# Optimization experiments

Hardware: AMD Instinct MI355X
Metric: run time of the kernel (lower is better)

## Reference

```python
import jax, jax.numpy as jnp
import numpy as np

TEMPERATURE = 0.6


def setup_inputs() -> dict:
    key = jax.random.key(0)
    k1, k2, k3 = jax.random.split(key, 3)
    B, IN, OUT, C = 8192, 256, 32, 50
    x = jax.random.uniform(k1, (B, IN), dtype=jnp.float32)
    weight = jax.random.normal(k2, (C, OUT, IN), dtype=jnp.float32) * 0.05
    bias = jax.random.normal(k3, (C, 1, OUT), dtype=jnp.float32) * 0.05
    return {"x": x, "weight": weight, "bias": bias}


def reference(x, weight, bias):
    # gamma[c,i] = L1 norm of weight over out dim: sum_o |W[c,o,i]|
    gamma = jnp.sum(jnp.abs(weight), axis=1)            # [C, IN]
    alpha = jax.nn.softmax(gamma / TEMPERATURE, axis=1)  # [C, IN]
    alpha_norm = alpha / jnp.max(alpha, axis=1, keepdims=True)  # [C, IN]
    # gated input per class: [C, B, IN]
    xg = x[None, :, :] * alpha_norm[:, None, :]
    # per-class GEMM: y[c,b,o] = sum_i xg[c,b,i] * W[c,o,i]
    y = jnp.einsum('cbi,coi->cbo', xg, weight) + bias    # [C, B, OUT]
    return jnp.transpose(y, (1, 0, 2))                   # [B, C, OUT]
```

## Files before the change

### kernel.cpp

```cpp
#include <hip/hip_runtime.h>
#include <hip/hip_bf16.h>

typedef __bf16 bf16x8 __attribute__((ext_vector_type(8)));
typedef float  f32x4  __attribute__((ext_vector_type(4)));

#define B_ROWS 8192
#define IN_DIM 256
#define OUT_DIM 32
#define NCLS 50
#define INV_T (1.0f / 0.6f)

#define CVT_BLOCKS 1024
#define GBLOCKS 512

__device__ __forceinline__ void gload_lds16(const void* g, void* l) {
    __builtin_amdgcn_global_load_lds(
        (const __attribute__((address_space(1))) void*)g,
        (__attribute__((address_space(3))) void*)l, 16, 0, 0);
}

__global__ __launch_bounds__(256) void prep(const float* __restrict__ x,
                                            const float* __restrict__ w,
                                            __bf16* __restrict__ xb,
                                            __bf16* __restrict__ wb) {
    __shared__ float wm[4];
    int bid = blockIdx.x;
    if (bid < CVT_BLOCKS) {
        int i = (bid * 256 + threadIdx.x) * 8;
        float4 v0 = *reinterpret_cast<const float4*>(x + i);
        float4 v1 = *reinterpret_cast<const float4*>(x + i + 4);
        bf16x8 r;
        r[0] = (__bf16)v0.x; r[1] = (__bf16)v0.y; r[2] = (__bf16)v0.z; r[3] = (__bf16)v0.w;
        r[4] = (__bf16)v1.x; r[5] = (__bf16)v1.y; r[6] = (__bf16)v1.z; r[7] = (__bf16)v1.w;
        *reinterpret_cast<bf16x8*>(xb + i) = r;
    } else {
        int c = bid - CVT_BLOCKS;
        int i = threadIdx.x;
        const float* wc = w + (size_t)c * OUT_DIM * IN_DIM;
        float g = 0.f;
#pragma unroll
        for (int o = 0; o < OUT_DIM; ++o) g += fabsf(wc[o * IN_DIM + i]);
        float m = g;
#pragma unroll
        for (int s = 1; s < 64; s <<= 1) m = fmaxf(m, __shfl_xor(m, s));
        if ((threadIdx.x & 63) == 0) wm[threadIdx.x >> 6] = m;
        __syncthreads();
        m = fmaxf(fmaxf(wm[0], wm[1]), fmaxf(wm[2], wm[3]));
        float an = __expf((g - m) * INV_T);
        __bf16* wbc = wb + (size_t)c * OUT_DIM * IN_DIM;
#pragma unroll
        for (int o = 0; o < OUT_DIM; ++o)
            wbc[o * IN_DIM + i] = (__bf16)(wc[o * IN_DIM + i] * an);
    }
}

__global__ __launch_bounds__(256, 2) void gemm(const __bf16* __restrict__ xb,
                                               const __bf16* __restrict__ wb,
                                               const float* __restrict__ bias,
                                               float* __restrict__ out) {
    __shared__ __align__(16) char lds[4 * 2 * 8192];

    int bid = blockIdx.x;
    int p = (bid * 25) >> 9;
    int first = (p * GBLOCKS + 24) / 25;
    int next  = ((p + 1) * GBLOCKS + 24) / 25;
    int j = bid - first;
    int np = next - first;
    int u0 = (j * 128) / np;
    int u1 = ((j + 1) * 128) / np;
    int nch = u1 - u0;

    int c0 = p * 2;
    int lane = threadIdx.x & 63;
    int w4 = threadIdx.x >> 6;
    int l15 = lane & 15;
    int g = lane >> 4;
    int s31 = lane & 31;
    int lr = lane >> 5;

    char* Abuf0 = lds + w4 * 16384;
    char* Abuf1 = Abuf0 + 8192;

    const char* arows = (const char*)(xb + (size_t)(u0 * 64 + w4 * 16) * IN_DIM);
#define STAGE_A(BUF, AP)                                                          \
    _Pragma("unroll") for (int il = 0; il < 8; ++il) {                            \
        int r = 2 * il + lr;                                                      \
        gload_lds16((AP) + (size_t)r * 512 + ((s31 ^ r) * 16),                    \
                    (BUF) + il * 1024);                                           \
    }
    STAGE_A(Abuf0, arows)

    const char* wsrc = (const char*)(wb + (size_t)c0 * OUT_DIM * IN_DIM);
#pragma unroll
    for (int jw = 0; jw < 8; ++jw) {
        int re = jw * 8 + w4 * 2;
        int r = re + lr;
        gload_lds16(wsrc + (size_t)r * 512 + ((s31 ^ (r & 15)) * 16),
                    lds + (re >> 4) * 16384 + 8192 + (re & 15) * 512);
    }

    asm volatile("s_waitcnt vmcnt(0)" ::: "memory");
    __syncthreads();
    __builtin_amdgcn_sched_barrier(0);

    bf16x8 W[2][16];
#pragma unroll
    for (int ci = 0; ci < 2; ++ci)
#pragma unroll
        for (int kk = 0; kk < 8; ++kk) {
            int slot = (4 * kk + g) ^ l15;
            W[ci][kk]     = *reinterpret_cast<const bf16x8*>(
                lds + (2 * ci) * 16384 + 8192 + l15 * 512 + slot * 16);
            W[ci][8 + kk] = *reinterpret_cast<const bf16x8*>(
                lds + (2 * ci + 1) * 16384 + 8192 + l15 * 512 + slot * 16);
        }
#pragma unroll
    for (int ci = 0; ci < 2; ++ci)
#pragma unroll
        for (int kk = 0; kk < 16; ++kk)
            asm volatile("" : "+v"(W[ci][kk]));
    __builtin_amdgcn_sched_barrier(0);
    __syncthreads();

    float4 bv00 = *reinterpret_cast<const float4*>(bias + c0 * OUT_DIM + g * 4);
    float4 bv01 = *reinterpret_cast<const float4*>(bias + c0 * OUT_DIM + 16 + g * 4);
    float4 bv10 = *reinterpret_cast<const float4*>(bias + (c0 + 1) * OUT_DIM + g * 4);
    float4 bv11 = *reinterpret_cast<const float4*>(bias + (c0 + 1) * OUT_DIM + 16 + g * 4);

    float* orow = out + (size_t)(u0 * 64 + w4 * 16 + l15) * (NCLS * OUT_DIM) + c0 * OUT_DIM + g * 4;

    char* cur = Abuf0;
    char* nxt = Abuf1;
    const char* anext = arows + 64 * 512;

    for (int k = 0; k < nch; ++k) {
        if (k + 1 < nch) {
            STAGE_A(nxt, anext)
            asm volatile("s_waitcnt vmcnt(12)" ::: "memory");
        } else {
            asm volatile("s_waitcnt vmcnt(4)" ::: "memory");
        }
        __builtin_amdgcn_sched_barrier(0);

        f32x4 acc00 = {bv00.x, bv00.y, bv00.z, bv00.w};
        f32x4 acc01 = {bv01.x, bv01.y, bv01.z, bv01.w};
        f32x4 acc10 = {bv10.x, bv10.y, bv10.z, bv10.w};
        f32x4 acc11 = {bv11.x, bv11.y, bv11.z, bv11.w};
#pragma unroll
        for (int kk = 0; kk < 8; ++kk) {
            int slot = (4 * kk + g) ^ l15;
            bf16x8 a = *reinterpret_cast<const bf16x8*>(cur + (size_t)l15 * 512 + slot * 16);
            acc00 = __builtin_amdgcn_mfma_f32_16x16x32_bf16(W[0][kk],     a, acc00, 0, 0, 0);
            acc01 = __builtin_amdgcn_mfma_f32_16x16x32_bf16(W[0][8 + kk], a, acc01, 0, 0, 0);
            acc10 = __builtin_amdgcn_mfma_f32_16x16x32_bf16(W[1][kk],     a, acc10, 0, 0, 0);
            acc11 = __builtin_amdgcn_mfma_f32_16x16x32_bf16(W[1][8 + kk], a, acc11, 0, 0, 0);
        }
        *reinterpret_cast<f32x4*>(orow) = acc00;
        *reinterpret_cast<f32x4*>(orow + 16) = acc01;
        *reinterpret_cast<f32x4*>(orow + OUT_DIM) = acc10;
        *reinterpret_cast<f32x4*>(orow + OUT_DIM + 16) = acc11;

        char* t = cur; cur = nxt; nxt = t;
        anext += 64 * 512;
        orow += (size_t)64 * (NCLS * OUT_DIM);
    }
#undef STAGE_A
}

extern "C" void kernel_launch(void* const* d_in, const int* in_sizes, int n_in,
                              void* d_out, int out_size, void* d_ws, size_t ws_size,
                              hipStream_t stream) {
    const float* x    = (const float*)d_in[0];
    const float* w    = (const float*)d_in[1];
    const float* bias = (const float*)d_in[2];
    float* out = (float*)d_out;

    __bf16* xb = (__bf16*)d_ws;
    __bf16* wb = xb + (size_t)B_ROWS * IN_DIM;

    prep<<<CVT_BLOCKS + NCLS, 256, 0, stream>>>(x, w, xb, wb);
    gemm<<<GBLOCKS, 256, 0, stream>>>(xb, wb, bias, out);
}
```

Measured before the change: 32.83 us.

## Load weights directly to registers and prefetch two A tiles up front

The prep kernel now schedules the weight-gating blocks first so they start early, and it loads each weight column into registers once instead of reading it twice. The GEMM kernel loads its weight fragments straight from global memory into registers, which removes the LDS staging round trip and two block barriers. It also issues the first two A-tile prefetches before the first compute, so more loads overlap with the MFMA work. The risk is that uncoalesced per-lane weight loads and higher register pressure could offset these savings.

```diff
diff --git a/kernel.cpp b/kernel.cpp
--- a/kernel.cpp
+++ b/kernel.cpp
@@ -25,32 +25,35 @@
                                             __bf16* __restrict__ wb) {
     __shared__ float wm[4];
     int bid = blockIdx.x;
-    if (bid < CVT_BLOCKS) {
-        int i = (bid * 256 + threadIdx.x) * 8;
+    if (bid < NCLS) {
+        int c = bid;
+        int i = threadIdx.x;
+        const float* wc = w + (size_t)c * OUT_DIM * IN_DIM + i;
+        float wv[OUT_DIM];
+#pragma unroll
+        for (int o = 0; o < OUT_DIM; ++o) wv[o] = wc[o * IN_DIM];
+        float gsum = 0.f;
+#pragma unroll
+        for (int o = 0; o < OUT_DIM; ++o) gsum += fabsf(wv[o]);
+        float m = gsum;
+#pragma unroll
+        for (int s = 1; s < 64; s <<= 1) m = fmaxf(m, __shfl_xor(m, s));
+        if ((threadIdx.x & 63) == 0) wm[threadIdx.x >> 6] = m;
+        __syncthreads();
+        m = fmaxf(fmaxf(wm[0], wm[1]), fmaxf(wm[2], wm[3]));
+        float an = __expf((gsum - m) * INV_T);
+        __bf16* wo = wb + (size_t)c * OUT_DIM * IN_DIM + i;
+#pragma unroll
+        for (int o = 0; o < OUT_DIM; ++o)
+            wo[o * IN_DIM] = (__bf16)(wv[o] * an);
+    } else {
+        int i = ((bid - NCLS) * 256 + threadIdx.x) * 8;
         float4 v0 = *reinterpret_cast<const float4*>(x + i);
         float4 v1 = *reinterpret_cast<const float4*>(x + i + 4);
         bf16x8 r;
         r[0] = (__bf16)v0.x; r[1] = (__bf16)v0.y; r[2] = (__bf16)v0.z; r[3] = (__bf16)v0.w;
         r[4] = (__bf16)v1.x; r[5] = (__bf16)v1.y; r[6] = (__bf16)v1.z; r[7] = (__bf16)v1.w;
         *reinterpret_cast<bf16x8*>(xb + i) = r;
-    } else {
-        int c = bid - CVT_BLOCKS;
-        int i = threadIdx.x;
-        const float* wc = w + (size_t)c * OUT_DIM * IN_DIM;
-        float g = 0.f;
-#pragma unroll
-        for (int o = 0; o < OUT_DIM; ++o) g += fabsf(wc[o * IN_DIM + i]);
-        float m = g;
-#pragma unroll
-        for (int s = 1; s < 64; s <<= 1) m = fmaxf(m, __shfl_xor(m, s));
-        if ((threadIdx.x & 63) == 0) wm[threadIdx.x >> 6] = m;
-        __syncthreads();
-        m = fmaxf(fmaxf(wm[0], wm[1]), fmaxf(wm[2], wm[3]));
-        float an = __expf((g - m) * INV_T);
-        __bf16* wbc = wb + (size_t)c * OUT_DIM * IN_DIM;
-#pragma unroll
-        for (int o = 0; o < OUT_DIM; ++o)
-            wbc[o * IN_DIM + i] = (__bf16)(wc[o * IN_DIM + i] * an);
     }
 }
 
@@ -81,6 +84,29 @@
     char* Abuf0 = lds + w4 * 16384;
     char* Abuf1 = Abuf0 + 8192;
 
+    const __bf16* wp = wb + ((size_t)c0 * OUT_DIM + l15) * IN_DIM + g * 8;
+    bf16x8 W[2][16];
+#pragma unroll
+    for (int ci = 0; ci < 2; ++ci)
+#pragma unroll
+        for (int kk = 0; kk < 8; ++kk) {
+            W[ci][kk]     = *reinterpret_cast<const bf16x8*>(wp + ci * 32 * IN_DIM + kk * 32);
+            W[ci][8 + kk] = *reinterpret_cast<const bf16x8*>(wp + (ci * 32 + 16) * IN_DIM + kk * 32);
+        }
+    f32x4 bv00 = *reinterpret_cast<const f32x4*>(bias + c0 * OUT_DIM + g * 4);
+    f32x4 bv01 = *reinterpret_cast<const f32x4*>(bias + c0 * OUT_DIM + 16 + g * 4);
+    f32x4 bv10 = *reinterpret_cast<const f32x4*>(bias + (c0 + 1) * OUT_DIM + g * 4);
+    f32x4 bv11 = *reinterpret_cast<const f32x4*>(bias + (c0 + 1) * OUT_DIM + 16 + g * 4);
+
+#pragma unroll
+    for (int ci = 0; ci < 2; ++ci)
+#pragma unroll
+        for (int kk = 0; kk < 16; ++kk)
+            asm volatile("" : "+v"(W[ci][kk]));
+    asm volatile("" : "+v"(bv00), "+v"(bv01), "+v"(bv10), "+v"(bv11));
+    asm volatile("s_waitcnt vmcnt(0)" ::: "memory");
+    __builtin_amdgcn_sched_barrier(0);
+
     const char* arows = (const char*)(xb + (size_t)(u0 * 64 + w4 * 16) * IN_DIM);
 #define STAGE_A(BUF, AP)                                                          \
     _Pragma("unroll") for (int il = 0; il < 8; ++il) {                            \
@@ -88,83 +114,54 @@
         gload_lds16((AP) + (size_t)r * 512 + ((s31 ^ r) * 16),                    \
                     (BUF) + il * 1024);                                           \
     }
+
     STAGE_A(Abuf0, arows)
+    float* orow = out + (size_t)(u0 * 64 + w4 * 16 + l15) * (NCLS * OUT_DIM) + c0 * OUT_DIM + g * 4;
 
-    const char* wsrc = (const char*)(wb + (size_t)c0 * OUT_DIM * IN_DIM);
-#pragma unroll
-    for (int jw = 0; jw < 8; ++jw) {
-        int re = jw * 8 + w4 * 2;
-        int r = re + lr;
-        gload_lds16(wsrc + (size_t)r * 512 + ((s31 ^ (r & 15)) * 16),
-                    lds + (re >> 4) * 16384 + 8192 + (re & 15) * 512);
+#define COMPUTE_STORE(BUF)                                                        \
+    {                                                                             \
+        f32x4 acc00 = bv00;                                                       \
+        f32x4 acc01 = bv01;                                                       \
+        f32x4 acc10 = bv10;                                                       \
+        f32x4 acc11 = bv11;                                                       \
+        _Pragma("unroll") for (int kk = 0; kk < 8; ++kk) {                        \
+            int slot = (4 * kk + g) ^ l15;                                        \
+            bf16x8 a = *reinterpret_cast<const bf16x8*>((BUF) + (size_t)l15 * 512 + slot * 16); \
+            acc00 = __builtin_amdgcn_mfma_f32_16x16x32_bf16(W[0][kk],     a, acc00, 0, 0, 0);   \
+            acc01 = __builtin_amdgcn_mfma_f32_16x16x32_bf16(W[0][8 + kk], a, acc01, 0, 0, 0);   \
+            acc10 = __builtin_amdgcn_mfma_f32_16x16x32_bf16(W[1][kk],     a, acc10, 0, 0, 0);   \
+            acc11 = __builtin_amdgcn_mfma_f32_16x16x32_bf16(W[1][8 + kk], a, acc11, 0, 0, 0);   \
+        }                                                                         \
+        *reinterpret_cast<f32x4*>(orow) = acc00;                                  \
+        *reinterpret_cast<f32x4*>(orow + 16) = acc01;                             \
+        *reinterpret_cast<f32x4*>(orow + OUT_DIM) = acc10;                        \
+        *reinterpret_cast<f32x4*>(orow + OUT_DIM + 16) = acc11;                   \
+        orow += (size_t)64 * (NCLS * OUT_DIM);                                    \
     }
 
-    asm volatile("s_waitcnt vmcnt(0)" ::: "memory");
-    __syncthreads();
+    STAGE_A(Abuf1, arows + 64 * 512)
+    asm volatile("s_waitcnt vmcnt(8)" ::: "memory");
     __builtin_amdgcn_sched_barrier(0);
+    COMPUTE_STORE(Abuf0)
 
-    bf16x8 W[2][16];
-#pragma unroll
-    for (int ci = 0; ci < 2; ++ci)
-#pragma unroll
-        for (int kk = 0; kk < 8; ++kk) {
-            int slot = (4 * kk + g) ^ l15;
-            W[ci][kk]     = *reinterpret_cast<const bf16x8*>(
-                lds + (2 * ci) * 16384 + 8192 + l15 * 512 + slot * 16);
-            W[ci][8 + kk] = *reinterpret_cast<const bf16x8*>(
-                lds + (2 * ci + 1) * 16384 + 8192 + l15 * 512 + slot * 16);
-        }
-#pragma unroll
-    for (int ci = 0; ci < 2; ++ci)
-#pragma unroll
-        for (int kk = 0; kk < 16; ++kk)
-            asm volatile("" : "+v"(W[ci][kk]));
-    __builtin_amdgcn_sched_barrier(0);
-    __syncthreads();
+    char* cur = Abuf1;
+    char* nxt = Abuf0;
+    const char* anext = arows + 2 * 64 * 512;
 
-    float4 bv00 = *reinterpret_cast<const float4*>(bias + c0 * OUT_DIM + g * 4);
-    float4 bv01 = *reinterpret_cast<const float4*>(bias + c0 * OUT_DIM + 16 + g * 4);
-    float4 bv10 = *reinterpret_cast<const float4*>(bias + (c0 + 1) * OUT_DIM + g * 4);
-    float4 bv11 = *reinterpret_cast<const float4*>(bias + (c0 + 1) * OUT_DIM + 16 + g * 4);
-
-    float* orow = out + (size_t)(u0 * 64 + w4 * 16 + l15) * (NCLS * OUT_DIM) + c0 * OUT_DIM + g * 4;
-
-    char* cur = Abuf0;
-    char* nxt = Abuf1;
-    const char* anext = arows + 64 * 512;
-
-    for (int k = 0; k < nch; ++k) {
+    for (int k = 1; k < nch; ++k) {
         if (k + 1 < nch) {
             STAGE_A(nxt, anext)
+            anext += 64 * 512;
             asm volatile("s_waitcnt vmcnt(12)" ::: "memory");
         } else {
             asm volatile("s_waitcnt vmcnt(4)" ::: "memory");
         }
         __builtin_amdgcn_sched_barrier(0);
-
-        f32x4 acc00 = {bv00.x, bv00.y, bv00.z, bv00.w};
-        f32x4 acc01 = {bv01.x, bv01.y, bv01.z, bv01.w};
-        f32x4 acc10 = {bv10.x, bv10.y, bv10.z, bv10.w};
-        f32x4 acc11 = {bv11.x, bv11.y, bv11.z, bv11.w};
-#pragma unroll
-        for (int kk = 0; kk < 8; ++kk) {
-            int slot = (4 * kk + g) ^ l15;
-            bf16x8 a = *reinterpret_cast<const bf16x8*>(cur + (size_t)l15 * 512 + slot * 16);
-            acc00 = __builtin_amdgcn_mfma_f32_16x16x32_bf16(W[0][kk],     a, acc00, 0, 0, 0);
-            acc01 = __builtin_amdgcn_mfma_f32_16x16x32_bf16(W[0][8 + kk], a, acc01, 0, 0, 0);
-            acc10 = __builtin_amdgcn_mfma_f32_16x16x32_bf16(W[1][kk],     a, acc10, 0, 0, 0);
-            acc11 = __builtin_amdgcn_mfma_f32_16x16x32_bf16(W[1][8 + kk], a, acc11, 0, 0, 0);
-        }
-        *reinterpret_cast<f32x4*>(orow) = acc00;
-        *reinterpret_cast<f32x4*>(orow + 16) = acc01;
-        *reinterpret_cast<f32x4*>(orow + OUT_DIM) = acc10;
-        *reinterpret_cast<f32x4*>(orow + OUT_DIM + 16) = acc11;
-
+        COMPUTE_STORE(cur)
         char* t = cur; cur = nxt; nxt = t;
-        anext += 64 * 512;
-        orow += (size_t)64 * (NCLS * OUT_DIM);
     }
 #undef STAGE_A
+#undef COMPUTE_STORE
 }
 
 extern "C" void kernel_launch(void* const* d_in, const int* in_sizes, int n_in,
@@ -178,6 +175,6 @@
     __bf16* xb = (__bf16*)d_ws;
     __bf16* wb = xb + (size_t)B_ROWS * IN_DIM;
 
-    prep<<<CVT_BLOCKS + NCLS, 256, 0, stream>>>(x, w, xb, wb);
+    prep<<<NCLS + CVT_BLOCKS, 256, 0, stream>>>(x, w, xb, wb);
     gemm<<<GBLOCKS, 256, 0, stream>>>(xb, wb, bias, out);
 }
```

Result: slower. 38.50 us (+17.2%).
